# Performance work log

Hardware: AMD Instinct MI355X
Metric: run time of the kernel (lower is better)

Reference implementation:

```python
import jax, jax.numpy as jnp
import numpy as np

N, L, G, NB = 1024, 30, 10000, 64  # cells, latent, genes, n_batch

def setup_inputs() -> dict:
    key = jax.random.key(0)
    k = jax.random.split(key, 7)
    z = jax.random.normal(k[0], (N, L), dtype=jnp.float32)
    batch_covariate = jax.random.randint(k[1], (N,), 0, NB, dtype=jnp.int32)
    size_factor = jax.random.uniform(k[2], (N, 1), dtype=jnp.float32)
    # learned params
    W_amat = jax.random.normal(k[3], (L, G), dtype=jnp.float32) * 0.05   # Dense(n_out, use_bias=False)
    A_emb = jax.random.normal(k[4], (NB, G, L), dtype=jnp.float32) * 0.05  # Embed(n_batch, n_out*n_in)
    b_emb = jax.random.normal(k[5], (NB, G), dtype=jnp.float32) * 0.05     # Embed(n_batch, n_out)
    px_r = jax.random.normal(k[6], (G,), dtype=jnp.float32)                # param 'px_r'
    return {"z": z, "batch_covariate": batch_covariate, "size_factor": size_factor,
            "W_amat": W_amat, "A_emb": A_emb, "b_emb": b_emb, "px_r": px_r}

def reference(z, batch_covariate, size_factor, W_amat, A_emb, b_emb, px_r):
    # h1 = Dense(n_out, no bias)(z)
    h1 = z @ W_amat                                  # [N, G]
    # dropout is deterministic (training=False) -> identity; stop_gradient as in source
    z_drop = jax.lax.stop_gradient(z)                # [N, L]
    idx = batch_covariate.astype(jnp.int32).reshape(-1)
    A_b = A_emb[idx]                                 # [N, G, L] per-sample gathered matrix
    h2 = jnp.einsum('cgl,cl->cg', A_b, z_drop)       # [N, G]
    h3 = b_emb[idx]                                  # [N, G]
    mu = jax.nn.softplus(h1 + h2 + h3)               # activation = nn.softplus
    mean = mu * size_factor                          # NegativeBinomial mean
    inverse_dispersion = jnp.exp(px_r)               # NegativeBinomial inverse_dispersion
    return mean, inverse_dispersion
```

## Files before the change

### kernel.cpp

```cpp
#include <hip/hip_runtime.h>

#define NCELLS 1024
#define LDIM   30
#define GDIM   10000
#define NBATCH 64
#define GPB    256
#define CH     64

typedef unsigned int  u32;

__global__ __launch_bounds__(256) void decoder_kernel(
    const float* __restrict__ z,
    const void*  __restrict__ cand1,
    const void*  __restrict__ cand2,
    const float* __restrict__ W,
    const float* __restrict__ A,
    const float* __restrict__ Bb,
    const float* __restrict__ px,
    float* __restrict__ out)
{
    const int b   = blockIdx.x;
    const int tid = threadIdx.x;
    const int gb  = blockIdx.y * GPB;
    const int g   = gb + tid;

    __shared__ __align__(16) float smem[GPB * LDIM];
    __shared__ int cells[NCELLS];
    __shared__ int cnt;

    bool c1_is_int = true;
    for (int i = 0; i < 64; i++)
        if (((const u32*)cand1)[i] >= 64u) { c1_is_int = false; break; }
    const int*   bcov = c1_is_int ? (const int*)cand1   : (const int*)cand2;
    const float* sf   = c1_is_int ? (const float*)cand2 : (const float*)cand1;

    if (tid == 0) cnt = 0;
    __syncthreads();
    for (int i = tid; i < NCELLS; i += 256)
        if (bcov[i] == b) cells[atomicAdd(&cnt, 1)] = i;

    const size_t abase = ((size_t)b * GDIM + gb) * LDIM;
    const size_t atot  = (size_t)NBATCH * GDIM * LDIM;
    float4* smem4 = (float4*)smem;
    for (int i = tid; i < GPB * LDIM / 4; i += 256) {
        size_t idx = abase + (size_t)i * 4;
        float4 v = make_float4(0.f, 0.f, 0.f, 0.f);
        if (idx + 4 <= atot) v = *(const float4*)(A + idx);
        smem4[i] = v;
    }
    __syncthreads();

    float M[LDIM];
    float h3 = 0.f;
    const bool valid = (g < GDIM);
    if (valid) {
        #pragma unroll
        for (int l = 0; l < LDIM; l++) M[l] = smem[tid * LDIM + l];
        #pragma unroll
        for (int l = 0; l < LDIM; l++) M[l] += W[l * GDIM + g];
        h3 = Bb[(size_t)b * GDIM + g];
        if (b == 0) out[(size_t)NCELLS * GDIM + g] = __expf(px[g]);
    }
    const int total = cnt;
    __syncthreads();

    float* z_sh  = smem;
    float* sf_sh = smem + CH * LDIM;
    for (int c0 = 0; c0 < total; c0 += CH) {
        const int nc = min(CH, total - c0);
        for (int i = tid; i < nc * LDIM; i += 256) {
            int cc = i / LDIM, l = i - cc * LDIM;
            z_sh[i] = z[(size_t)cells[c0 + cc] * LDIM + l];
        }
        for (int i = tid; i < nc; i += 256)
            sf_sh[i] = sf[cells[c0 + i]];
        __syncthreads();

        if (valid) {
            for (int cc = 0; cc < nc; cc++) {
                float acc = h3;
                #pragma unroll
                for (int l = 0; l < LDIM; l++)
                    acc = fmaf(M[l], z_sh[cc * LDIM + l], acc);
                float sp = fmaxf(acc, 0.f) + log1pf(__expf(-fabsf(acc)));
                out[(size_t)cells[c0 + cc] * GDIM + g] = sp * sf_sh[cc];
            }
        }
        __syncthreads();
    }
}

extern "C" void kernel_launch(void* const* d_in, const int* in_sizes, int n_in,
                              void* d_out, int out_size, void* d_ws, size_t ws_size,
                              hipStream_t stream) {
    const float* z  = nullptr;
    const float* W  = nullptr;
    const float* A  = nullptr;
    const float* Bb = nullptr;
    const float* px = nullptr;
    const void*  p1024[2] = {nullptr, nullptr};
    int n1024 = 0;
    for (int i = 0; i < n_in; i++) {
        switch (in_sizes[i]) {
            case NCELLS * LDIM:        z  = (const float*)d_in[i]; break;
            case LDIM * GDIM:          W  = (const float*)d_in[i]; break;
            case NBATCH * GDIM * LDIM: A  = (const float*)d_in[i]; break;
            case NBATCH * GDIM:        Bb = (const float*)d_in[i]; break;
            case GDIM:                 px = (const float*)d_in[i]; break;
            case NCELLS:
                if (n1024 < 2) p1024[n1024] = d_in[i];
                n1024++;
                break;
            default: break;
        }
    }
    if (!z || !W || !A || !Bb || !px || n1024 != 2) {
        z  = (const float*)d_in[0];
        p1024[0] = d_in[1];
        p1024[1] = d_in[2];
        W  = (const float*)d_in[3];
        A  = (const float*)d_in[4];
        Bb = (const float*)d_in[5];
        px = (const float*)d_in[6];
    }
    float* out = (float*)d_out;

    decoder_kernel<<<dim3(NBATCH, (GDIM + GPB - 1) / GPB), 256, 0, stream>>>(
        z, p1024[0], p1024[1], W, A, Bb, px, out);
}
```

Baseline: 190.0 us.

## Read z directly via wave-uniform scalar loads instead of staged LDS chunks

```diff
diff --git a/kernel.cpp b/kernel.cpp
--- a/kernel.cpp
+++ b/kernel.cpp
@@ -5,11 +5,10 @@
 #define GDIM   10000
 #define NBATCH 64
 #define GPB    256
-#define CH     64
 
-typedef unsigned int  u32;
+typedef unsigned int u32;
 
-__global__ __launch_bounds__(256) void decoder_kernel(
+__global__ __launch_bounds__(256, 4) void decoder_kernel(
     const float* __restrict__ z,
     const void*  __restrict__ cand1,
     const void*  __restrict__ cand2,
@@ -24,7 +23,7 @@
     const int gb  = blockIdx.y * GPB;
     const int g   = gb + tid;
 
-    __shared__ __align__(16) float smem[GPB * LDIM];
+    __shared__ __align__(16) float a_sh[GPB * LDIM];
     __shared__ int cells[NCELLS];
     __shared__ int cnt;
 
@@ -41,52 +40,65 @@
 
     const size_t abase = ((size_t)b * GDIM + gb) * LDIM;
     const size_t atot  = (size_t)NBATCH * GDIM * LDIM;
-    float4* smem4 = (float4*)smem;
+    float4* a4 = (float4*)a_sh;
     for (int i = tid; i < GPB * LDIM / 4; i += 256) {
         size_t idx = abase + (size_t)i * 4;
         float4 v = make_float4(0.f, 0.f, 0.f, 0.f);
         if (idx + 4 <= atot) v = *(const float4*)(A + idx);
-        smem4[i] = v;
+        a4[i] = v;
     }
     __syncthreads();
 
+    const int total = cnt;
+    if (g >= GDIM) return;
+
     float M[LDIM];
-    float h3 = 0.f;
-    const bool valid = (g < GDIM);
-    if (valid) {
+    {
+        const float2* ar = (const float2*)(a_sh + tid * LDIM);
         #pragma unroll
-        for (int l = 0; l < LDIM; l++) M[l] = smem[tid * LDIM + l];
+        for (int j = 0; j < LDIM / 2; j++) {
+            float2 w = ar[j];
+            M[2*j]   = w.x + W[(2*j)   * GDIM + g];
+            M[2*j+1] = w.y + W[(2*j+1) * GDIM + g];
+        }
+    }
+    const float h3 = Bb[(size_t)b * GDIM + g];
+    if (b == 0) out[(size_t)NCELLS * GDIM + g] = __expf(px[g]);
+
+    int c = 0;
+    for (; c + 2 <= total; c += 2) {
+        const int cell0 = __builtin_amdgcn_readfirstlane(cells[c]);
+        const int cell1 = __builtin_amdgcn_readfirstlane(cells[c + 1]);
+        const float* z0 = z + (size_t)cell0 * LDIM;
+        const float* z1 = z + (size_t)cell1 * LDIM;
+        const float s0 = sf[cell0], s1 = sf[cell1];
+        float a0 = h3, b0 = 0.f, a1 = h3, b1 = 0.f;
         #pragma unroll
-        for (int l = 0; l < LDIM; l++) M[l] += W[l * GDIM + g];
-        h3 = Bb[(size_t)b * GDIM + g];
-        if (b == 0) out[(size_t)NCELLS * GDIM + g] = __expf(px[g]);
+        for (int l = 0; l < LDIM; l += 2) {
+            a0 = fmaf(M[l],     z0[l],     a0);
+            b0 = fmaf(M[l + 1], z0[l + 1], b0);
+            a1 = fmaf(M[l],     z1[l],     a1);
+            b1 = fmaf(M[l + 1], z1[l + 1], b1);
+        }
+        float x0 = a0 + b0, x1 = a1 + b1;
+        float p0 = fmaxf(x0, 0.f) + __logf(1.f + __expf(-fabsf(x0)));
+        float p1 = fmaxf(x1, 0.f) + __logf(1.f + __expf(-fabsf(x1)));
+        out[(size_t)cell0 * GDIM + g] = p0 * s0;
+        out[(size_t)cell1 * GDIM + g] = p1 * s1;
     }
-    const int total = cnt;
-    __syncthreads();
-
-    float* z_sh  = smem;
-    float* sf_sh = smem + CH * LDIM;
-    for (int c0 = 0; c0 < total; c0 += CH) {
-        const int nc = min(CH, total - c0);
-        for (int i = tid; i < nc * LDIM; i += 256) {
-            int cc = i / LDIM, l = i - cc * LDIM;
-            z_sh[i] = z[(size_t)cells[c0 + cc] * LDIM + l];
+    if (c < total) {
+        const int cell0 = __builtin_amdgcn_readfirstlane(cells[c]);
+        const float* z0 = z + (size_t)cell0 * LDIM;
+        const float s0 = sf[cell0];
+        float a0 = h3, b0 = 0.f;
+        #pragma unroll
+        for (int l = 0; l < LDIM; l += 2) {
+            a0 = fmaf(M[l],     z0[l],     a0);
+            b0 = fmaf(M[l + 1], z0[l + 1], b0);
         }
-        for (int i = tid; i < nc; i += 256)
-            sf_sh[i] = sf[cells[c0 + i]];
-        __syncthreads();
-
-        if (valid) {
-            for (int cc = 0; cc < nc; cc++) {
-                float acc = h3;
-                #pragma unroll
-                for (int l = 0; l < LDIM; l++)
-                    acc = fmaf(M[l], z_sh[cc * LDIM + l], acc);
-                float sp = fmaxf(acc, 0.f) + log1pf(__expf(-fabsf(acc)));
-                out[(size_t)cells[c0 + cc] * GDIM + g] = sp * sf_sh[cc];
-            }
-        }
-        __syncthreads();
+        float x0 = a0 + b0;
+        float p0 = fmaxf(x0, 0.f) + __logf(1.f + __expf(-fabsf(x0)));
+        out[(size_t)cell0 * GDIM + g] = p0 * s0;
     }
 }
 
```

Result: faster. 172.6 us (-9.2%).
